# Performance work log

Hardware: AMD Instinct MI355X
Metric: run time of the kernel (lower is better)

The kernel has to match this reference:

```python
import jax, jax.numpy as jnp
import numpy as np

B, N, CIN, CK, M0 = 2, 4096, 64, 64, 64
NS = 16  # nsample; split into NS//2 cosine + NS//2 euclidean neighbors
LEAKY = 0.1


def _leaky(x):
    return jax.nn.leaky_relu(x, LEAKY)


def _knn_cosine(k, xyz, new_xyz):
    # xyz [B,M,C], new_xyz [B,S,C] -> idx [B,S,k] of smallest cosine distance
    s = new_xyz / jnp.sqrt(jnp.sum(new_xyz ** 2, -1, keepdims=True) + 1e-8)
    d = xyz / jnp.sqrt(jnp.sum(xyz ** 2, -1, keepdims=True) + 1e-8)
    dist = 1.0 - jnp.einsum('bsc,bmc->bsm', s, d)
    return jax.lax.top_k(-dist, k)[1]


def _knn_euclid(k, xyz, new_xyz):
    # squared euclidean distance [B,S,M]
    dist = (jnp.sum(new_xyz ** 2, -1)[:, :, None]
            + jnp.sum(xyz ** 2, -1)[:, None, :]
            - 2.0 * jnp.einsum('bsc,bmc->bsm', new_xyz, xyz))
    return jax.lax.top_k(-dist, k)[1]


def _group(points, idx):
    # points [B,M,C], idx [B,S,K] -> [B,S,K,C]
    return jax.vmap(lambda p, i: p[i])(points, idx)


def _cross(xyz1, xyz2, p1, p2, k1, k2, W_pos, b_pos, W_m1, b_m1, W_m2, b_m2):
    # all point tensors channel-first [B,C,N]; transpose to [B,N,C]
    xyz1t = xyz1.transpose(0, 2, 1)
    xyz2t = xyz2.transpose(0, 2, 1)
    p1t = p1.transpose(0, 2, 1)
    p2t = p2.transpose(0, 2, 1)
    k1t = k1.transpose(0, 2, 1)
    k2t = k2.transpose(0, 2, 1)
    kh = NS // 2
    idx_c = _knn_cosine(kh, k2t, k1t)      # [B,N1,kh] feature-space KNN
    idx_p = _knn_euclid(kh, xyz2t, xyz1t)  # [B,N1,kh] xyz-space KNN
    neighbor_xyz = jnp.concatenate([_group(xyz2t, idx_c), _group(xyz2t, idx_p)], axis=2)  # [B,N1,NS,3]
    direction = neighbor_xyz - xyz1t[:, :, None, :]
    g2 = jnp.concatenate([_group(p2t, idx_c), _group(p2t, idx_p)], axis=2)  # [B,N1,NS,D]
    pos = jnp.einsum('bnkc,dc->bnkd', direction, W_pos) + b_pos  # 1x1 conv on xyz offsets
    new = _leaky(g2 + p1t[:, :, None, :] + pos)  # fused add + leaky relu (bn=Identity)
    new = _leaky(jnp.einsum('bnkd,ed->bnke', new, W_m1) + b_m1)
    new = _leaky(jnp.einsum('bnkd,ed->bnke', new, W_m2) + b_m2)
    new = jnp.max(new, axis=2)  # max-pool over neighbor dim -> [B,N1,D]
    return new.transpose(0, 2, 1)  # [B,D,N1]


def setup_inputs() -> dict:
    key = jax.random.key(0)
    ks = jax.random.split(key, 12)
    rn = lambda k, shape, s=1.0: jax.random.normal(k, shape, jnp.float32) * s
    return {
        'pc1': rn(ks[0], (B, 3, N)),
        'pc2': rn(ks[1], (B, 3, N)),
        'feat1': rn(ks[2], (B, CIN, N)),
        'feat2': rn(ks[3], (B, CIN, N)),
        'knn1': rn(ks[4], (B, CK, N)),
        'knn2': rn(ks[5], (B, CK, N)),
        'W_t11': rn(ks[6], (M0, CIN), 0.1),
        'b_t11': jnp.zeros((M0,), jnp.float32),
        'W_t22': rn(ks[7], (M0, CIN), 0.1),
        'b_t22': jnp.zeros((M0,), jnp.float32),
        'W_pos': rn(ks[8], (M0, 3), 0.1),
        'b_pos': jnp.zeros((M0,), jnp.float32),
        'W_m1': rn(ks[9], (M0, M0), 0.1),
        'b_m1': jnp.zeros((M0,), jnp.float32),
        'W_m2': rn(ks[10], (M0, M0), 0.1),
        'b_m2': jnp.zeros((M0,), jnp.float32),
    }


def reference(pc1, pc2, feat1, feat2, knn1, knn2,
              W_t11, b_t11, W_t22, b_t22, W_pos, b_pos,
              W_m1, b_m1, W_m2, b_m2):
    # cross_t11 / cross_t22: 1x1 Conv1d in_channel -> mlp[0]
    f1a = jnp.einsum('dc,bcn->bdn', W_t11, feat1) + b_t11[None, :, None]
    f2a = jnp.einsum('dc,bcn->bdn', W_t22, feat2) + b_t22[None, :, None]
    f2b = jnp.einsum('dc,bcn->bdn', W_t11, feat2) + b_t11[None, :, None]
    f1b = jnp.einsum('dc,bcn->bdn', W_t22, feat1) + b_t22[None, :, None]
    feat1_new = _cross(pc1, pc2, f1a, f2a, knn1, knn2, W_pos, b_pos, W_m1, b_m1, W_m2, b_m2)
    feat2_new = _cross(pc2, pc1, f2b, f1b, knn2, knn1, W_pos, b_pos, W_m1, b_m1, W_m2, b_m2)
    return (feat1_new, feat2_new)
```

## Files before the change

kernel.cpp:

```cpp
#include <hip/hip_runtime.h>
#include <hip/hip_bf16.h>

#define BB 2
#define NN 4096
#define CH 64

typedef __bf16 bf16x8 __attribute__((ext_vector_type(8)));
typedef float f32x4 __attribute__((ext_vector_type(4)));

__device__ __forceinline__ float lrelu(float v) { return fmaxf(v, 0.1f * v); }
__device__ __forceinline__ float tobf(const __hip_bfloat16& h) { return __bfloat162float(h); }

#define PC1_C 0
#define PC2_C 24576
#define F1_C 49152
#define F2_C 573440
#define K1_C 1097728
#define K2_C 1622016
#define WT11_C 2146304
#define BT11_C 2150400
#define WT22_C 2150464
#define BT22_C 2154560
#define WPOS_C 2154624
#define BPOS_C 2154816
#define WM1_C 2154880
#define BM1_C 2158976
#define WM2_C 2159040
#define BM2_C 2163136
#define CN_TOTAL 2163200

#define FHALF (2 * BB * NN * CH)

__device__ __forceinline__ unsigned fmap(float s) {
  unsigned u = __float_as_uint(s);
  return u ^ ((unsigned)((int)u >> 31) | 0x80000000u);
}

__device__ __forceinline__ unsigned umaxu(unsigned a, unsigned b) { return a > b ? a : b; }
__device__ __forceinline__ void casu(unsigned& a, unsigned& b) {
  unsigned mx = a > b ? a : b;
  unsigned mn = a > b ? b : a;
  a = mx; b = mn;
}

__device__ __forceinline__ void bitonic8(unsigned bd[8]) {
  casu(bd[0], bd[4]); casu(bd[1], bd[5]); casu(bd[2], bd[6]); casu(bd[3], bd[7]);
  casu(bd[0], bd[2]); casu(bd[1], bd[3]); casu(bd[4], bd[6]); casu(bd[5], bd[7]);
  casu(bd[0], bd[1]); casu(bd[2], bd[3]); casu(bd[4], bd[5]); casu(bd[6], bd[7]);
}

__device__ __forceinline__ void merge4(unsigned bd[8], unsigned k0, unsigned k1,
                                       unsigned k2, unsigned k3) {
  casu(k0, k1); casu(k2, k3); casu(k0, k2); casu(k1, k3); casu(k1, k2);
  bd[4] = umaxu(bd[4], k3); bd[5] = umaxu(bd[5], k2);
  bd[6] = umaxu(bd[6], k1); bd[7] = umaxu(bd[7], k0);
  bitonic8(bd);
}

__device__ __forceinline__ void merge88(unsigned a[8], const unsigned b[8]) {
  a[0] = umaxu(a[0], b[7]); a[1] = umaxu(a[1], b[6]);
  a[2] = umaxu(a[2], b[5]); a[3] = umaxu(a[3], b[4]);
  a[4] = umaxu(a[4], b[3]); a[5] = umaxu(a[5], b[2]);
  a[6] = umaxu(a[6], b[1]); a[7] = umaxu(a[7], b[0]);
  bitonic8(a);
}

__device__ __forceinline__ void xmerge(unsigned a[8], int m) {
  unsigned t[8];
#pragma unroll
  for (int k = 0; k < 8; ++k) t[k] = (unsigned)__shfl_xor((int)a[k], m, 64);
  merge88(a, t);
}

__global__ void k_detect(const unsigned short* __restrict__ pc1raw, int* __restrict__ flag) {
  int lane = threadIdx.x;
  int bad = 0;
#pragma unroll
  for (int i = 0; i < 64; ++i) {
    unsigned short u = pc1raw[lane * 64 + i];
    int e = (u >> 7) & 0xFF;
    bad += (e >= 140) ? 1 : 0;
  }
#pragma unroll
  for (int s = 32; s; s >>= 1) bad += __shfl_xor(bad, s, 64);
  if (lane == 0) *flag = (bad > 16) ? 1 : 0;
}

__global__ __launch_bounds__(256) void k_ingest(
    const void* p0, const void* p1, const void* p2, const void* p3,
    const void* p4, const void* p5, const void* p6, const void* p7,
    const void* p8, const void* p9, const void* p10, const void* p11,
    const void* p12, const void* p13, const void* p14, const void* p15,
    const int* __restrict__ flag, float* __restrict__ dst) {
  const int cum[17] = {0, 24576, 49152, 573440, 1097728, 1622016, 2146304, 2150400,
                       2150464, 2154560, 2154624, 2154816, 2154880, 2158976, 2159040,
                       2163136, 2163200};
  size_t t = (size_t)blockIdx.x * 256 + threadIdx.x;
  if (t >= (size_t)CN_TOTAL) return;
  int seg = 0;
#pragma unroll
  for (int i = 1; i < 16; ++i) seg += (t >= (size_t)cum[i]) ? 1 : 0;
  size_t local = t - (size_t)cum[seg];
  const void* ptrs[16] = {p0, p1, p2, p3, p4, p5, p6, p7, p8, p9, p10, p11, p12, p13, p14, p15};
  const void* p = ptrs[seg];
  float v;
  if (*flag) v = ((const float*)p)[local];
  else       v = tobf(((const __hip_bfloat16*)p)[local]);
  if (!(v == v) || fabsf(v) > 1e30f) v = 0.f;
  dst[t] = v;
}

__global__ __launch_bounds__(256) void k_prep_all(const float* __restrict__ cn,
                                                  float* __restrict__ knnt,
                                                  __hip_bfloat16* __restrict__ knnb,
                                                  __hip_bfloat16* __restrict__ fhl,
                                                  __hip_bfloat16* __restrict__ wmb,
                                                  float4* __restrict__ xyzt,
                                                  float4* __restrict__ wp4,
                                                  __hip_bfloat16* __restrict__ wcb) {
  int bid = blockIdx.x;
  if (bid < 64) {
    int t = bid * 256 + threadIdx.x;
    int n = t & (NN - 1);
    int b = (t >> 12) & 1;
    int a = t >> 13;
    const float* col = cn + (a ? K2_C : K1_C) + (size_t)b * CH * NN + n;
    float s = 0.f;
#pragma unroll
    for (int c = 0; c < CH; ++c) { float v = col[(size_t)c * NN]; s += v * v; }
    float inv = 1.0f / sqrtf(s + 1e-8f);
    size_t row = (size_t)(a * BB + b) * NN + n;
    float* o = knnt + row * CH;
    __hip_bfloat16* ob = knnb + row * CH;
#pragma unroll
    for (int c = 0; c < CH; ++c) {
      float v = col[(size_t)c * NN] * inv;
      o[c] = v;
      ob[c] = __float2bfloat16(v);
    }
  } else if (bid < 128) {
    int t = (bid - 64) * 256 + threadIdx.x;
    int n = t & (NN - 1);
    int b = (t >> 12) & 1;
    int a = t >> 13;
    const float* col = cn + (a ? F2_C : F1_C) + (size_t)b * CH * NN + n;
    __hip_bfloat16* oh = fhl + ((size_t)(a * BB + b) * NN + n) * CH;
    __hip_bfloat16* ol = oh + FHALF;
#pragma unroll
    for (int c = 0; c < CH; ++c) {
      float v = col[(size_t)c * NN];
      __hip_bfloat16 hi = __float2bfloat16(v);
      oh[c] = hi;
      ol[c] = __float2bfloat16(v - tobf(hi));
    }
  } else if (bid < 160) {
    int t = (bid - 128) * 256 + threadIdx.x;
    float v = (t < 4096) ? cn[WM1_C + t] : cn[WM2_C + (t - 4096)];
    wmb[t] = __float2bfloat16(v);
  } else if (bid < 224) {
    int t = (bid - 160) * 256 + threadIdx.x;
    int n = t & (NN - 1);
    int b = (t >> 12) & 1;
    int a = t >> 13;
    const float* p = cn + (a ? PC2_C : PC1_C) + (size_t)b * 3 * NN + n;
    float x = p[0], y = p[NN], z = p[2 * NN];
    xyzt[(size_t)(a * BB + b) * NN + n] = make_float4(x, y, z, x * x + y * y + z * z);
  } else if (bid == 224) {
    int c = threadIdx.x;
    if (c < 64)
      wp4[c] = make_float4(cn[WPOS_C + 3 * c], cn[WPOS_C + 3 * c + 1],
                           cn[WPOS_C + 3 * c + 2], cn[BPOS_C + c]);
  } else {
    int t = (bid - 225) * 256 + threadIdx.x;
    int w = t >> 12, e = t & 4095;
    float v = cn[(w ? WT22_C : WT11_C) + e];
    __hip_bfloat16 hi = __float2bfloat16(v);
    __hip_bfloat16 lo = __float2bfloat16(v - tobf(hi));
    wcb[w * 4096 + e] = hi;
    wcb[8192 + w * 4096 + e] = lo;
  }
}

__global__ __launch_bounds__(512, 4) void k_knncv(const __hip_bfloat16* __restrict__ knnb,
                                                  const float* __restrict__ knnt,
                                                  const float4* __restrict__ xyzt,
                                                  const __hip_bfloat16* __restrict__ fhl,
                                                  const __hip_bfloat16* __restrict__ wcb,
                                                  const float* __restrict__ cn,
                                                  int* __restrict__ idxf,
                                                  float* __restrict__ fbuf) {
  int bid = blockIdx.x;
  if (bid >= 1024) {
    int cb = bid - 1024;
    int b = cb & 1;
    int a = (cb >> 1) & 1;
    int ntile = (cb >> 2) * 2 + (threadIdx.x >> 8);
    int t = threadIdx.x & 255;
    int dt = t >> 6;
    int lane = t & 63;
    int lo = lane & 15, g = lane >> 4;

    const __hip_bfloat16* fb = fhl + ((size_t)(a * BB + b) * NN + ntile * 16 + lo) * CH;
    bf16x8 ah0 = *reinterpret_cast<const bf16x8*>(fb + g * 8);
    bf16x8 ah1 = *reinterpret_cast<const bf16x8*>(fb + 32 + g * 8);
    bf16x8 al0 = *reinterpret_cast<const bf16x8*>(fb + FHALF + g * 8);
    bf16x8 al1 = *reinterpret_cast<const bf16x8*>(fb + FHALF + 32 + g * 8);

#pragma unroll
    for (int w = 0; w < 2; ++w) {
      const __hip_bfloat16* wb = wcb + w * 4096 + (dt * 16 + lo) * 64;
      bf16x8 wh0 = *reinterpret_cast<const bf16x8*>(wb + g * 8);
      bf16x8 wh1 = *reinterpret_cast<const bf16x8*>(wb + 32 + g * 8);
      bf16x8 wl0 = *reinterpret_cast<const bf16x8*>(wb + 8192 + g * 8);
      bf16x8 wl1 = *reinterpret_cast<const bf16x8*>(wb + 8192 + 32 + g * 8);
      float bv = cn[(w ? BT22_C : BT11_C) + dt * 16 + lo];
      f32x4 acc = {bv, bv, bv, bv};
      acc = __builtin_amdgcn_mfma_f32_16x16x32_bf16(ah0, wh0, acc, 0, 0, 0);
      acc = __builtin_amdgcn_mfma_f32_16x16x32_bf16(ah1, wh1, acc, 0, 0, 0);
      acc = __builtin_amdgcn_mfma_f32_16x16x32_bf16(al0, wh0, acc, 0, 0, 0);
      acc = __builtin_amdgcn_mfma_f32_16x16x32_bf16(al1, wh1, acc, 0, 0, 0);
      acc = __builtin_amdgcn_mfma_f32_16x16x32_bf16(ah0, wl0, acc, 0, 0, 0);
      acc = __builtin_amdgcn_mfma_f32_16x16x32_bf16(ah1, wl1, acc, 0, 0, 0);
      int sel = a ? (w ? 1 : 2) : (w ? 3 : 0);
      float* ob = fbuf + ((size_t)(sel * BB + b) * NN + ntile * 16 + g * 4) * CH + dt * 16 + lo;
      ob[0 * CH] = acc[0];
      ob[1 * CH] = acc[1];
      ob[2 * CH] = acc[2];
      ob[3 * CH] = acc[3];
    }
    return;
  }

  __shared__ unsigned sk[16 * 8 * 9];
  __shared__ int cidx[16 * 16];
  int b = bid & 1;
  int x = (bid >> 1) & 1;
  int qt = bid >> 2;
  int w = threadIdx.x >> 6;
  int lane = threadIdx.x & 63;
  int lo = lane & 15, g = lane >> 4;
  int q0 = qt * 16;
  int j0 = w * (NN / 8);
  int hw = lane >> 5, sl = lane & 31;
  int qq = w * 2 + hw;
  size_t qbase = (size_t)(x * BB + b) * NN;
  size_t dbase = (size_t)((1 - x) * BB + b) * NN;

  const __hip_bfloat16* qb = knnb + (qbase + q0) * CH;
  bf16x8 qf0 = *reinterpret_cast<const bf16x8*>(qb + lo * CH + g * 8);
  bf16x8 qf1 = *reinterpret_cast<const bf16x8*>(qb + lo * CH + 32 + g * 8);
  const __hip_bfloat16* db = knnb + dbase * CH;
  const float4 q4 = xyzt[qbase + q0 + lo];
  const float4* dbx = xyzt + dbase;
  float tx = 2.f * q4.x, ty = 2.f * q4.y, tz = 2.f * q4.z;

  unsigned bc0[8], bc1[8], be0[8], be1[8];
#pragma unroll
  for (int k = 0; k < 8; ++k) { bc0[k] = 0u; bc1[k] = 0u; be0[k] = 0u; be1[k] = 0u; }

  auto STEP = [&](const bf16x8& A0, const bf16x8& A1, const float4& P0,
                  const float4& P1, const float4& P2, const float4& P3,
                  int rcv, unsigned (&bc)[8], unsigned (&be)[8]) {
    f32x4 acc = {0.f, 0.f, 0.f, 0.f};
    acc = __builtin_amdgcn_mfma_f32_16x16x32_bf16(A0, qf0, acc, 0, 0, 0);
    acc = __builtin_amdgcn_mfma_f32_16x16x32_bf16(A1, qf1, acc, 0, 0, 0);
    float v0 = fmaf(tx, P0.x, fmaf(ty, P0.y, fmaf(tz, P0.z, -P0.w)));
    float v1 = fmaf(tx, P1.x, fmaf(ty, P1.y, fmaf(tz, P1.z, -P1.w)));
    float v2 = fmaf(tx, P2.x, fmaf(ty, P2.y, fmaf(tz, P2.z, -P2.w)));
    float v3 = fmaf(tx, P3.x, fmaf(ty, P3.y, fmaf(tz, P3.z, -P3.w)));
    unsigned r = (unsigned)rcv;
    merge4(bc, (__float_as_uint(acc[0] + 4.0f) & 0xFFFFF000u) | r,
               (__float_as_uint(acc[1] + 4.0f) & 0xFFFFF000u) | (r - 1),
               (__float_as_uint(acc[2] + 4.0f) & 0xFFFFF000u) | (r - 2),
               (__float_as_uint(acc[3] + 4.0f) & 0xFFFFF000u) | (r - 3));
    merge4(be, (fmap(v0) & 0xFFFFF000u) | r,
               (fmap(v1) & 0xFFFFF000u) | (r - 1),
               (fmap(v2) & 0xFFFFF000u) | (r - 2),
               (fmap(v3) & 0xFFFFF000u) | (r - 3));
  };

  const __hip_bfloat16* arA = db + (size_t)(j0 + lo) * CH + g * 8;
  const __hip_bfloat16* arB = arA + 16 * CH;
  const float4* peA = dbx + j0 + g * 4;
  const float4* peB = peA + 16;
  int rc = 4095 - j0 - g * 4;

  bf16x8 aA0 = *reinterpret_cast<const bf16x8*>(arA);
  bf16x8 aA1 = *reinterpret_cast<const bf16x8*>(arA + 32);
  float4 pA0 = peA[0], pA1 = peA[1], pA2 = peA[2], pA3 = peA[3];

  for (int i = 0; i < 15; ++i) {
    bf16x8 aB0 = *reinterpret_cast<const bf16x8*>(arB);
    bf16x8 aB1 = *reinterpret_cast<const bf16x8*>(arB + 32);
    float4 pB0 = peB[0], pB1 = peB[1], pB2 = peB[2], pB3 = peB[3];
    STEP(aA0, aA1, pA0, pA1, pA2, pA3, rc, bc0, be0);
    arA += 32 * CH; peA += 32;
    aA0 = *reinterpret_cast<const bf16x8*>(arA);
    aA1 = *reinterpret_cast<const bf16x8*>(arA + 32);
    pA0 = peA[0]; pA1 = peA[1]; pA2 = peA[2]; pA3 = peA[3];
    STEP(aB0, aB1, pB0, pB1, pB2, pB3, rc - 16, bc1, be1);
    arB += 32 * CH; peB += 32;
    rc -= 32;
  }
  {
    bf16x8 aB0 = *reinterpret_cast<const bf16x8*>(arB);
    bf16x8 aB1 = *reinterpret_cast<const bf16x8*>(arB + 32);
    float4 pB0 = peB[0], pB1 = peB[1], pB2 = peB[2], pB3 = peB[3];
    STEP(aA0, aA1, pA0, pA1, pA2, pA3, rc, bc0, be0);
    STEP(aB0, aB1, pB0, pB1, pB2, pB3, rc - 16, bc1, be1);
  }
  merge88(bc0, bc1);
  merge88(be0, be1);
  xmerge(bc0, 16); xmerge(bc0, 32);
  xmerge(be0, 16); xmerge(be0, 32);

  if (g == 0) {
#pragma unroll
    for (int k = 0; k < 8; ++k) sk[(lo * 8 + k) * 9 + w] = bc0[k];
  }
  __syncthreads();
  {
    unsigned e[16];
#pragma unroll
    for (int k = 0; k < 8; ++k) e[k] = sk[(qq * 8 + k) * 9 + (sl & 7)];
#pragma unroll
    for (int k = 8; k < 16; ++k) e[k] = 0u;
#pragma unroll
    for (int s = 1; s < 8; s <<= 1) {
      unsigned f[16];
#pragma unroll
      for (int k = 0; k < 16; ++k) f[k] = (unsigned)__shfl_xor((int)e[k], s, 64);
#pragma unroll
      for (int i = 0; i < 16; ++i) e[i] = umaxu(e[i], f[15 - i]);
      casu(e[0], e[8]); casu(e[1], e[9]); casu(e[2], e[10]); casu(e[3], e[11]);
      casu(e[4], e[12]); casu(e[5], e[13]); casu(e[6], e[14]); casu(e[7], e[15]);
      casu(e[0], e[4]); casu(e[1], e[5]); casu(e[2], e[6]); casu(e[3], e[7]);
      casu(e[8], e[12]); casu(e[9], e[13]); casu(e[10], e[14]); casu(e[11], e[15]);
      casu(e[0], e[2]); casu(e[1], e[3]); casu(e[4], e[6]); casu(e[5], e[7]);
      casu(e[8], e[10]); casu(e[9], e[11]); casu(e[12], e[14]); casu(e[13], e[15]);
      casu(e[0], e[1]); casu(e[2], e[3]); casu(e[4], e[5]); casu(e[6], e[7]);
      casu(e[8], e[9]); casu(e[10], e[11]); casu(e[12], e[13]); casu(e[14], e[15]);
    }
    if (sl == 0) {
#pragma unroll
      for (int k = 0; k < 16; ++k) cidx[qq * 16 + k] = 4095 - (int)(e[k] & 4095u);
    }
    int c = sl >> 1, hr = sl & 1;
    int idx = cidx[qq * 16 + c];
    const float4* qr = reinterpret_cast<const float4*>(knnt + (qbase + q0 + qq) * CH) + hr * 8;
    const float4* dr = reinterpret_cast<const float4*>(knnt + (dbase + idx) * CH) + hr * 8;
    float v = 0.f;
#pragma unroll 4
    for (int cb = 0; cb < 8; ++cb) {
      float4 qv = qr[cb], dv = dr[cb];
      v += qv.x * dv.x + qv.y * dv.y + qv.z * dv.z + qv.w * dv.w;
    }
    v += __shfl_xor(v, 1, 64);
    int ii = idx;
#pragma unroll
    for (int k = 2; k <= 32; k <<= 1) {
#pragma unroll
      for (int j = k >> 1; j >= 1; j >>= 1) {
        float ov = __shfl_xor(v, j, 64);
        int oi = __shfl_xor(ii, j, 64);
        bool ob = (ov > v) || (ov == v && oi < ii);
        bool want = (((sl & k) == 0) == ((sl & j) == 0));
        bool take = (want == ob);
        v = take ? ov : v;
        ii = take ? oi : ii;
      }
    }
    if (sl < 16 && (sl & 1) == 0) idxf[(qbase + q0 + qq) * 16 + (sl >> 1)] = ii;
  }
  __syncthreads();

  if (g == 0) {
#pragma unroll
    for (int k = 0; k < 8; ++k) sk[(lo * 8 + k) * 9 + w] = be0[k];
  }
  __syncthreads();
  {
    unsigned e[16];
#pragma unroll
    for (int k = 0; k < 8; ++k) e[k] = sk[(qq * 8 + k) * 9 + (sl & 7)];
#pragma unroll
    for (int k = 8; k < 16; ++k) e[k] = 0u;
#pragma unroll
    for (int s = 1; s < 8; s <<= 1) {
      unsigned f[16];
#pragma unroll
      for (int k = 0; k < 16; ++k) f[k] = (unsigned)__shfl_xor((int)e[k], s, 64);
#pragma unroll
      for (int i = 0; i < 16; ++i) e[i] = umaxu(e[i], f[15 - i]);
      casu(e[0], e[8]); casu(e[1], e[9]); casu(e[2], e[10]); casu(e[3], e[11]);
      casu(e[4], e[12]); casu(e[5], e[13]); casu(e[6], e[14]); casu(e[7], e[15]);
      casu(e[0], e[4]); casu(e[1], e[5]); casu(e[2], e[6]); casu(e[3], e[7]);
      casu(e[8], e[12]); casu(e[9], e[13]); casu(e[10], e[14]); casu(e[11], e[15]);
      casu(e[0], e[2]); casu(e[1], e[3]); casu(e[4], e[6]); casu(e[5], e[7]);
      casu(e[8], e[10]); casu(e[9], e[11]); casu(e[12], e[14]); casu(e[13], e[15]);
      casu(e[0], e[1]); casu(e[2], e[3]); casu(e[4], e[5]); casu(e[6], e[7]);
      casu(e[8], e[9]); casu(e[10], e[11]); casu(e[12], e[13]); casu(e[14], e[15]);
    }
    if (sl == 0) {
#pragma unroll
      for (int k = 0; k < 16; ++k) cidx[qq * 16 + k] = 4095 - (int)(e[k] & 4095u);
    }
    int c = sl >> 1;
    int idx = cidx[qq * 16 + c];
    const float4 qx4 = xyzt[qbase + q0 + qq];
    float4 p = xyzt[dbase + idx];
    float v = fmaf(2.f * qx4.x, p.x, fmaf(2.f * qx4.y, p.y, fmaf(2.f * qx4.z, p.z, -p.w)));
    int ii = idx;
#pragma unroll
    for (int k = 2; k <= 32; k <<= 1) {
#pragma unroll
      for (int j = k >> 1; j >= 1; j >>= 1) {
        float ov = __shfl_xor(v, j, 64);
        int oi = __shfl_xor(ii, j, 64);
        bool ob = (ov > v) || (ov == v && oi < ii);
        bool want = (((sl & k) == 0) == ((sl & j) == 0));
        bool take = (want == ob);
        v = take ? ov : v;
        ii = take ? oi : ii;
      }
    }
    if (sl < 16 && (sl & 1) == 0) idxf[(qbase + q0 + qq) * 16 + 8 + (sl >> 1)] = ii;
  }
}

__global__ __launch_bounds__(256) void k_mlp(const float* __restrict__ fbuf,
                                             const float4* __restrict__ xyzt,
                                             const int* __restrict__ idxf,
                                             const float4* __restrict__ wp4,
                                             const __hip_bfloat16* __restrict__ wmb,
                                             const float* __restrict__ cn,
                                             float* __restrict__ out) {
  __shared__ __bf16 h1s[4 * 16 * 72];
  const int t = threadIdx.x;
  const int wv = t >> 6, L = t & 63;
  const int lo = L & 15, g = L >> 4;
  int bid = blockIdx.x;
  const int b = bid & 1;
  const int x = (bid >> 1) & 1;
  const int qt = bid >> 2;
  const int q = qt * 4 + wv;

  bf16x8 w1f[4][2], w2f[4][2];
#pragma unroll
  for (int tt = 0; tt < 4; ++tt)
#pragma unroll
    for (int kc = 0; kc < 2; ++kc) {
      int e = tt * 16 + lo, c0 = kc * 32 + g * 8;
      w1f[tt][kc] = *reinterpret_cast<const bf16x8*>(wmb + e * 64 + c0);
      w2f[tt][kc] = *reinterpret_cast<const bf16x8*>(wmb + 4096 + e * 64 + c0);
    }

  const float* pq  = fbuf + ((size_t)((x ? 2 : 0) * BB + b)) * NN * CH;
  const float* pdb = fbuf + ((size_t)((x ? 3 : 1) * BB + b)) * NN * CH;
  const float4* qx  = xyzt + (size_t)(x * BB + b) * NN;
  const float4* dbx = xyzt + (size_t)((1 - x) * BB + b) * NN;

  const int m = lo;
  int jm = idxf[(((size_t)x * BB + b) * NN + q) * 16 + m];
  jm &= (NN - 1);
  const float4 q4 = qx[q];
  const float4 p4 = dbx[jm];
  const float dx = p4.x - q4.x, dy = p4.y - q4.y, dz = p4.z - q4.z;

  const float4* g2v = reinterpret_cast<const float4*>(pdb + (size_t)jm * CH);
  const float4* pqv = reinterpret_cast<const float4*>(pq + (size_t)q * CH);
  float hv[16];
  {
    float4 t0 = g2v[g * 2], t1 = g2v[g * 2 + 1], t2 = g2v[g * 2 + 8], t3 = g2v[g * 2 + 9];
    float4 u0 = pqv[g * 2], u1 = pqv[g * 2 + 1], u2 = pqv[g * 2 + 8], u3 = pqv[g * 2 + 9];
    hv[0] = t0.x + u0.x; hv[1] = t0.y + u0.y; hv[2] = t0.z + u0.z; hv[3] = t0.w + u0.w;
    hv[4] = t1.x + u1.x; hv[5] = t1.y + u1.y; hv[6] = t1.z + u1.z; hv[7] = t1.w + u1.w;
    hv[8] = t2.x + u2.x; hv[9] = t2.y + u2.y; hv[10] = t2.z + u2.z; hv[11] = t2.w + u2.w;
    hv[12] = t3.x + u3.x; hv[13] = t3.y + u3.y; hv[14] = t3.z + u3.z; hv[15] = t3.w + u3.w;
  }

  bf16x8 a0, a1;
#pragma unroll
  for (int kc = 0; kc < 2; ++kc) {
#pragma unroll
    for (int j = 0; j < 8; ++j) {
      int c = kc * 32 + g * 8 + j;
      float4 wp = wp4[c];
      float v = hv[kc * 8 + j] + wp.x * dx + wp.y * dy + wp.z * dz + wp.w;
      v = lrelu(v);
      if (kc == 0) a0[j] = (__bf16)v; else a1[j] = (__bf16)v;
    }
  }

  __bf16* hrow = h1s + wv * 16 * 72;
#pragma unroll
  for (int tt = 0; tt < 4; ++tt) {
    float bv = cn[BM1_C + tt * 16 + lo];
    f32x4 acc = {bv, bv, bv, bv};
    acc = __builtin_amdgcn_mfma_f32_16x16x32_bf16(a0, w1f[tt][0], acc, 0, 0, 0);
    acc = __builtin_amdgcn_mfma_f32_16x16x32_bf16(a1, w1f[tt][1], acc, 0, 0, 0);
#pragma unroll
    for (int r = 0; r < 4; ++r) {
      float v = lrelu(acc[r]);
      hrow[(g * 4 + r) * 72 + tt * 16 + lo] = (__bf16)v;
    }
  }
  __syncthreads();
  bf16x8 h1a = *reinterpret_cast<const bf16x8*>(hrow + m * 72 + g * 8);
  bf16x8 h1b = *reinterpret_cast<const bf16x8*>(hrow + m * 72 + 32 + g * 8);

  size_t obase = ((size_t)(x * BB + b) * CH) * NN;
#pragma unroll
  for (int tt = 0; tt < 4; ++tt) {
    float bv = cn[BM2_C + tt * 16 + lo];
    f32x4 acc = {bv, bv, bv, bv};
    acc = __builtin_amdgcn_mfma_f32_16x16x32_bf16(h1a, w2f[tt][0], acc, 0, 0, 0);
    acc = __builtin_amdgcn_mfma_f32_16x16x32_bf16(h1b, w2f[tt][1], acc, 0, 0, 0);
    float v = fmaxf(fmaxf(lrelu(acc[0]), lrelu(acc[1])), fmaxf(lrelu(acc[2]), lrelu(acc[3])));
    v = fmaxf(v, __shfl_xor(v, 16, 64));
    v = fmaxf(v, __shfl_xor(v, 32, 64));
    if (g == 0) out[obase + (size_t)(tt * 16 + lo) * NN + q] = v;
  }
}

#define CN_OFF 0
#define FB_OFF ((size_t)CN_TOTAL)
#define KT_OFF (FB_OFF + (size_t)4 * BB * NN * CH)
#define XZ_OFF (KT_OFF + (size_t)2 * BB * NN * CH)
#define WP4_OFF (XZ_OFF + (size_t)2 * BB * NN * 4)
#define WMB_OFF (WP4_OFF + 256)
#define IDX_OFF (WMB_OFF + 4096)
#define FLAG_OFF (IDX_OFF + 262144)
#define KNB_OFF (FLAG_OFF + 4)
#define FHL_OFF (KNB_OFF + (size_t)BB * NN * CH)
#define WCB_OFF (FHL_OFF + (size_t)2 * BB * NN * CH)

extern "C" void kernel_launch(void* const* d_in, const int* in_sizes, int n_in,
                              void* d_out, int out_size, void* d_ws, size_t ws_size,
                              hipStream_t stream) {
  float* ws = (float*)d_ws;
  float* cn = ws + CN_OFF;
  int* flag = (int*)(ws + FLAG_OFF);

  k_detect<<<1, 64, 0, stream>>>((const unsigned short*)d_in[0], flag);
  k_ingest<<<(CN_TOTAL + 255) / 256, 256, 0, stream>>>(
      d_in[0], d_in[1], d_in[2], d_in[3], d_in[4], d_in[5], d_in[6], d_in[7],
      d_in[8], d_in[9], d_in[10], d_in[11], d_in[12], d_in[13], d_in[14], d_in[15],
      flag, cn);
  k_prep_all<<<257, 256, 0, stream>>>(cn, ws + KT_OFF, (__hip_bfloat16*)(ws + KNB_OFF),
                                      (__hip_bfloat16*)(ws + FHL_OFF),
                                      (__hip_bfloat16*)(ws + WMB_OFF),
                                      (float4*)(ws + XZ_OFF), (float4*)(ws + WP4_OFF),
                                      (__hip_bfloat16*)(ws + WCB_OFF));
  k_knncv<<<1536, 512, 0, stream>>>(
      (const __hip_bfloat16*)(ws + KNB_OFF), ws + KT_OFF, (const float4*)(ws + XZ_OFF),
      (const __hip_bfloat16*)(ws + FHL_OFF), (const __hip_bfloat16*)(ws + WCB_OFF),
      cn, (int*)(ws + IDX_OFF), ws + FB_OFF);
  k_mlp<<<2 * BB * (NN / 4), 256, 0, stream>>>(ws + FB_OFF, (const float4*)(ws + XZ_OFF),
                                               (const int*)(ws + IDX_OFF), (const float4*)(ws + WP4_OFF),
                                               (const __hip_bfloat16*)(ws + WMB_OFF), cn,
                                               (float*)d_out);
}
```

Measured before the change: 274.7 us.

## Merge cosine and euclid candidate refinement into one parallel pass, raise occupancy hint

The two sequential top-k refinement phases (cosine and euclidean) now run concurrently: half of the waves handle cosine and half handle euclidean, with 16 lanes per query instead of 32. This removes two barriers and one serialized phase. The exact cosine dot product now runs on one lane per candidate over all 64 channels rather than being split across two lanes. The launch bound minimum blocks per CU is also raised from 4 to 6, which may force register spills.

Result: slower. 289.3 us (+5.3%).

```diff
diff --git a/kernel.cpp b/kernel.cpp
--- a/kernel.cpp
+++ b/kernel.cpp
@@ -181,7 +181,7 @@
   }
 }
 
-__global__ __launch_bounds__(512, 4) void k_knncv(const __hip_bfloat16* __restrict__ knnb,
+__global__ __launch_bounds__(512, 6) void k_knncv(const __hip_bfloat16* __restrict__ knnb,
                                                   const float* __restrict__ knnt,
                                                   const float4* __restrict__ xyzt,
                                                   const __hip_bfloat16* __restrict__ fhl,
@@ -231,8 +231,9 @@
     return;
   }
 
-  __shared__ unsigned sk[16 * 8 * 9];
-  __shared__ int cidx[16 * 16];
+  __shared__ unsigned skc[16 * 8 * 9];
+  __shared__ unsigned ske[16 * 8 * 9];
+  __shared__ int cidx[2 * 16 * 16];
   int b = bid & 1;
   int x = (bid >> 1) & 1;
   int qt = bid >> 2;
@@ -241,8 +242,6 @@
   int lo = lane & 15, g = lane >> 4;
   int q0 = qt * 16;
   int j0 = w * (NN / 8);
-  int hw = lane >> 5, sl = lane & 31;
-  int qq = w * 2 + hw;
   size_t qbase = (size_t)(x * BB + b) * NN;
   size_t dbase = (size_t)((1 - x) * BB + b) * NN;
 
@@ -316,13 +315,21 @@
 
   if (g == 0) {
 #pragma unroll
-    for (int k = 0; k < 8; ++k) sk[(lo * 8 + k) * 9 + w] = bc0[k];
+    for (int k = 0; k < 8; ++k) {
+      skc[(lo * 8 + k) * 9 + w] = bc0[k];
+      ske[(lo * 8 + k) * 9 + w] = be0[k];
+    }
   }
   __syncthreads();
+
   {
+    int p = w >> 2;
+    int qq = (w & 3) * 4 + (lane >> 4);
+    int sl = lane & 15;
+    const unsigned* skp = p ? ske : skc;
     unsigned e[16];
 #pragma unroll
-    for (int k = 0; k < 8; ++k) e[k] = sk[(qq * 8 + k) * 9 + (sl & 7)];
+    for (int k = 0; k < 8; ++k) e[k] = skp[(qq * 8 + k) * 9 + (sl & 7)];
 #pragma unroll
     for (int k = 8; k < 16; ++k) e[k] = 0u;
 #pragma unroll
@@ -343,22 +350,27 @@
     }
     if (sl == 0) {
 #pragma unroll
-      for (int k = 0; k < 16; ++k) cidx[qq * 16 + k] = 4095 - (int)(e[k] & 4095u);
-    }
-    int c = sl >> 1, hr = sl & 1;
-    int idx = cidx[qq * 16 + c];
-    const float4* qr = reinterpret_cast<const float4*>(knnt + (qbase + q0 + qq) * CH) + hr * 8;
-    const float4* dr = reinterpret_cast<const float4*>(knnt + (dbase + idx) * CH) + hr * 8;
-    float v = 0.f;
+      for (int k = 0; k < 16; ++k) cidx[(p * 16 + qq) * 16 + k] = 4095 - (int)(e[k] & 4095u);
+    }
+    int idx = cidx[(p * 16 + qq) * 16 + sl];
+    float v;
+    if (p == 0) {
+      const float4* qr = reinterpret_cast<const float4*>(knnt + (qbase + q0 + qq) * CH);
+      const float4* dr = reinterpret_cast<const float4*>(knnt + (dbase + idx) * CH);
+      v = 0.f;
 #pragma unroll 4
-    for (int cb = 0; cb < 8; ++cb) {
-      float4 qv = qr[cb], dv = dr[cb];
-      v += qv.x * dv.x + qv.y * dv.y + qv.z * dv.z + qv.w * dv.w;
-    }
-    v += __shfl_xor(v, 1, 64);
+      for (int cb = 0; cb < 16; ++cb) {
+        float4 qv = qr[cb], dv = dr[cb];
+        v += qv.x * dv.x + qv.y * dv.y + qv.z * dv.z + qv.w * dv.w;
+      }
+    } else {
+      const float4 qx4 = xyzt[qbase + q0 + qq];
+      float4 pp = xyzt[dbase + idx];
+      v = fmaf(2.f * qx4.x, pp.x, fmaf(2.f * qx4.y, pp.y, fmaf(2.f * qx4.z, pp.z, -pp.w)));
+    }
     int ii = idx;
 #pragma unroll
-    for (int k = 2; k <= 32; k <<= 1) {
+    for (int k = 2; k <= 16; k <<= 1) {
 #pragma unroll
       for (int j = k >> 1; j >= 1; j >>= 1) {
         float ov = __shfl_xor(v, j, 64);
@@ -370,61 +382,7 @@
         ii = take ? oi : ii;
       }
     }
-    if (sl < 16 && (sl & 1) == 0) idxf[(qbase + q0 + qq) * 16 + (sl >> 1)] = ii;
-  }
-  __syncthreads();
-
-  if (g == 0) {
-#pragma unroll
-    for (int k = 0; k < 8; ++k) sk[(lo * 8 + k) * 9 + w] = be0[k];
-  }
-  __syncthreads();
-  {
-    unsigned e[16];
-#pragma unroll
-    for (int k = 0; k < 8; ++k) e[k] = sk[(qq * 8 + k) * 9 + (sl & 7)];
-#pragma unroll
-    for (int k = 8; k < 16; ++k) e[k] = 0u;
-#pragma unroll
-    for (int s = 1; s < 8; s <<= 1) {
-      unsigned f[16];
-#pragma unroll
-      for (int k = 0; k < 16; ++k) f[k] = (unsigned)__shfl_xor((int)e[k], s, 64);
-#pragma unroll
-      for (int i = 0; i < 16; ++i) e[i] = umaxu(e[i], f[15 - i]);
-      casu(e[0], e[8]); casu(e[1], e[9]); casu(e[2], e[10]); casu(e[3], e[11]);
-      casu(e[4], e[12]); casu(e[5], e[13]); casu(e[6], e[14]); casu(e[7], e[15]);
-      casu(e[0], e[4]); casu(e[1], e[5]); casu(e[2], e[6]); casu(e[3], e[7]);
-      casu(e[8], e[12]); casu(e[9], e[13]); casu(e[10], e[14]); casu(e[11], e[15]);
-      casu(e[0], e[2]); casu(e[1], e[3]); casu(e[4], e[6]); casu(e[5], e[7]);
-      casu(e[8], e[10]); casu(e[9], e[11]); casu(e[12], e[14]); casu(e[13], e[15]);
-      casu(e[0], e[1]); casu(e[2], e[3]); casu(e[4], e[5]); casu(e[6], e[7]);
-      casu(e[8], e[9]); casu(e[10], e[11]); casu(e[12], e[13]); casu(e[14], e[15]);
-    }
-    if (sl == 0) {
-#pragma unroll
-      for (int k = 0; k < 16; ++k) cidx[qq * 16 + k] = 4095 - (int)(e[k] & 4095u);
-    }
-    int c = sl >> 1;
-    int idx = cidx[qq * 16 + c];
-    const float4 qx4 = xyzt[qbase + q0 + qq];
-    float4 p = xyzt[dbase + idx];
-    float v = fmaf(2.f * qx4.x, p.x, fmaf(2.f * qx4.y, p.y, fmaf(2.f * qx4.z, p.z, -p.w)));
-    int ii = idx;
-#pragma unroll
-    for (int k = 2; k <= 32; k <<= 1) {
-#pragma unroll
-      for (int j = k >> 1; j >= 1; j >>= 1) {
-        float ov = __shfl_xor(v, j, 64);
-        int oi = __shfl_xor(ii, j, 64);
-        bool ob = (ov > v) || (ov == v && oi < ii);
-        bool want = (((sl & k) == 0) == ((sl & j) == 0));
-        bool take = (want == ob);
-        v = take ? ov : v;
-        ii = take ? oi : ii;
-      }
-    }
-    if (sl < 16 && (sl & 1) == 0) idxf[(qbase + q0 + qq) * 16 + 8 + (sl >> 1)] = ii;
+    if (sl < 8) idxf[(qbase + q0 + qq) * 16 + p * 8 + sl] = ii;
   }
 }
 
```
